# Performance work log

Hardware: AMD Instinct MI355X
Metric: run time of the kernel (lower is better)

## Reference

```python
import jax, jax.numpy as jnp
import numpy as np

N = 50000      # nodes
E = 100000     # edges
D_IN = 16      # raw node feature dim
K = 16         # RWSE steps
H = 32         # node_hidden_dim (== D_IN + K for residual)
ED = H * H     # edge_input_dim, must be H*H for NNConv reshape


def _seg_sum(x, idx, n):
    return jax.ops.segment_sum(x, idx, num_segments=n)


def setup_inputs() -> dict:
    key = jax.random.key(0)
    ks = jax.random.split(key, 14)
    s = 0.02
    return {
        "n_feat": jax.random.normal(ks[0], (N, D_IN), jnp.float32),
        "e_feat": jax.random.normal(ks[1], (E, ED), jnp.float32),
        "src": jax.random.randint(ks[2], (E,), 0, N, jnp.int32),
        "dst": jax.random.randint(ks[3], (E,), 0, N, jnp.int32),
        "edge_proj_w": jax.random.normal(ks[4], (ED, ED), jnp.float32) * s,
        "edge_proj_b": jnp.zeros((ED,), jnp.float32),
        "gate_w": jax.random.normal(ks[5], (ED, 1), jnp.float32) * s,
        "gate_b": jnp.zeros((1,), jnp.float32),
        "lin0_w": jax.random.normal(ks[6], (D_IN + K, H), jnp.float32) * s,
        "lin0_b": jnp.zeros((H,), jnp.float32),
        "conv_bias": jnp.zeros((H,), jnp.float32),
        "message_w": jax.random.normal(ks[7], (2 * H, H), jnp.float32) * s,
        "message_b": jnp.zeros((H,), jnp.float32),
        "subgraph_w": jax.random.normal(ks[8], (2 * H, H), jnp.float32) * s,
        "subgraph_b": jnp.zeros((H,), jnp.float32),
    }


def reference(n_feat, e_feat, src, dst, edge_proj_w, edge_proj_b, gate_w, gate_b,
              lin0_w, lin0_b, conv_bias, message_w, message_b, subgraph_w, subgraph_b):
    ones_e = jnp.ones((E,), n_feat.dtype)
    deg = _seg_sum(ones_e, dst, N)                 # in-degree (adj row-sum)
    degc = jnp.where(deg == 0, 1.0, deg)

    # --- RWSE (sparse equivalent of dense adj @ x recursion) ---
    x = degc
    cols = [x]
    for _ in range(K - 1):
        x = _seg_sum(x[src], dst, N) / degc
        cols.append(x)
    rwse = jnp.stack(cols, axis=1)                 # (N, K)

    nf = jnp.concatenate([n_feat, rwse], axis=-1)  # (N, D_IN+K)
    init = nf
    out = jax.nn.relu(nf @ lin0_w + lin0_b)        # (N, H)

    # --- edge-conditioned weights (EnhancedEdgeNetwork), same every step ---
    proj = jax.nn.relu(e_feat @ edge_proj_w + edge_proj_b)   # (E, H*H)
    gate = jax.nn.sigmoid(e_feat @ gate_w + gate_b)          # (E, 1)
    W = (proj * gate).reshape(E, H, H)                       # (E, H, H)

    # --- NNConv mean-aggregation message passing (num_steps//2 iters) ---
    for _ in range(3):
        msg = jnp.einsum('eh,eho->eo', out[src], W)          # gather + transform
        neigh = _seg_sum(msg, dst, N) / degc[:, None]        # scatter-mean
        m = jax.nn.relu(neigh + out + conv_bias)             # residual (identity) + bias
        out = jnp.concatenate([m, out], axis=1) @ message_w + message_b

    # --- copy_u/mean group pooling + subgraph projection ---
    group = _seg_sum(out[src], dst, N) / degc[:, None]
    out = jnp.concatenate([out, group], axis=1) @ subgraph_w + subgraph_b
    return out + init
```

## Files before the change

kernel.cpp:

```cpp
#include <hip/hip_runtime.h>
#include <hip/hip_bf16.h>

typedef unsigned short u16;
typedef unsigned int   u32;
typedef __bf16 bf16x8 __attribute__((ext_vector_type(8)));
typedef float  f32x4  __attribute__((ext_vector_type(4)));

#define AS1 __attribute__((address_space(1)))
#define AS3 __attribute__((address_space(3)))

__device__ __forceinline__ u16 f2bf(float f){
    u32 u = __float_as_uint(f);
    u32 r = u + 0x7fffu + ((u>>16)&1u);
    return (u16)(r>>16);
}
__device__ __forceinline__ float bf2f(u16 u){ return __uint_as_float(((u32)u)<<16); }

__global__ void k_deg(const int* __restrict__ dst, float* __restrict__ degb, int E){
    int e = blockIdx.x*256 + threadIdx.x;
    if (e < E) atomicAdd(&degb[dst[e]], 1.0f);
}

__global__ void k_degc(float* __restrict__ invdeg, float* __restrict__ rw0, int n){
    int v = blockIdx.x*256 + threadIdx.x;
    if (v < n){
        float c = invdeg[v];
        if (c == 0.f) c = 1.f;
        invdeg[v] = 1.f/c;
        rw0[v] = c*c;
    }
}

__global__ void k_rwse(const float* __restrict__ cur, float* __restrict__ nxt,
                       const float* __restrict__ invdeg, const int* __restrict__ src,
                       const int* __restrict__ dst, int E){
    int e = blockIdx.x*256 + threadIdx.x;
    if (e < E){
        int s = src[e];
        atomicAdd(&nxt[dst[e]], cur[s]*invdeg[s]);
    }
}

__global__ void k_finalize(const float* __restrict__ nfeat, const float* __restrict__ rw,
                           const float* __restrict__ invdeg,
                           const float* __restrict__ lw, const float* __restrict__ lb,
                           float* __restrict__ out0, int n){
    __shared__ float lwl[1024];
    __shared__ float lbl[32];
    __shared__ float nfl[8][32];
    int tid = threadIdx.x;
    for (int i = tid; i < 1024; i += 256) lwl[i] = lw[i];
    if (tid < 32) lbl[tid] = lb[tid];
    int slot = tid>>5, o = tid&31;
    int v = blockIdx.x*8 + slot;
    float nfv = 0.f;
    if (v < n){
        nfv = (o < 16) ? nfeat[(size_t)v*16 + o]
                       : rw[(size_t)(o-16)*n + v]*invdeg[v];
    }
    nfl[slot][o] = nfv;
    __syncthreads();
    if (v < n){
        float a = lbl[o];
        #pragma unroll
        for (int j = 0; j < 32; j++) a += nfl[slot][j]*lwl[j*32+o];
        out0[(size_t)v*32 + o] = a > 0.f ? a : 0.f;
    }
}

__global__ void k_transpose(const float* __restrict__ w, u16* __restrict__ wt){
    __shared__ float t[32][33];
    int bx = blockIdx.x & 31, by = blockIdx.x >> 5;
    int x = threadIdx.x & 31, y = threadIdx.x >> 5;
    #pragma unroll
    for (int i = 0; i < 32; i += 8)
        t[y+i][x] = w[(size_t)(by*32 + y + i)*1024 + bx*32 + x];
    __syncthreads();
    #pragma unroll
    for (int i = 0; i < 32; i += 8)
        wt[(size_t)(bx*32 + y + i)*1024 + by*32 + x] = f2bf(t[x][y+i]);
}

__global__ __launch_bounds__(256) void k_prep(
    const float* __restrict__ A, const float* __restrict__ gw,
    const float* __restrict__ gb, u16* __restrict__ Abf,
    float* __restrict__ gate, int E)
{
    __shared__ f32x4 gwl[256];
    const int tid = threadIdx.x;
    const int wave = tid>>6, lane = tid&63;
    gwl[tid] = ((const f32x4*)gw)[tid];
    __syncthreads();
    const int row = blockIdx.x*4 + wave;
    if (row >= E) return;
    const f32x4* ar = (const f32x4*)(A + (size_t)row*1024);
    ushort4* br = (ushort4*)(Abf + (size_t)row*1024);
    float g = 0.f;
    #pragma unroll
    for (int j = 0; j < 4; j++){
        const int idx = j*64 + lane;
        f32x4 v = ar[idx];
        f32x4 w4 = gwl[idx];
        g += v.x*w4.x + v.y*w4.y + v.z*w4.z + v.w*w4.w;
        ushort4 o;
        o.x = f2bf(v.x); o.y = f2bf(v.y); o.z = f2bf(v.z); o.w = f2bf(v.w);
        br[idx] = o;
    }
    #pragma unroll
    for (int m = 32; m >= 1; m >>= 1) g += __shfl_xor(g, m);
    if (lane == 0) gate[row] = 1.f/(1.f + __expf(-(g + gb[0])));
}

__global__ __launch_bounds__(256) void k_gemm(
    const u16* __restrict__ A, const u16* __restrict__ BT,
    const float* __restrict__ bias, const float* __restrict__ gate,
    u16* __restrict__ Wout, int E)
{
    __shared__ __align__(16) u16 lds_a[3*128*32];
    __shared__ __align__(16) u16 lds_b[3*128*32];
    __shared__ float gate_lds[128];
    __shared__ float bias_lds[128];

    const int tid  = threadIdx.x;
    const int wave = tid>>6, lane = tid&63;
    const int wm = wave>>1, wn = wave&1;
    const int ql = lane>>4, rl = lane&15;

    const int id  = blockIdx.x;
    const int xcd = id & 7;
    const int s   = id >> 3;
    const int nb  = s & 7;
    const int mb  = (s >> 3)*8 + xcd;
    const int MBtot = (E + 127) >> 7;
    if (mb >= MBtot) return;
    const int m0 = mb<<7, n0 = nb<<7;

    if (tid < 128){
        const int row = m0 + tid;
        gate_lds[tid] = gate[row < E ? row : E-1];
    } else {
        bias_lds[tid-128] = bias[n0 + tid - 128];
    }
    __syncthreads();

    const int ci0 = (0*4 + wave)*64 + lane;
    const int ci1 = (1*4 + wave)*64 + lane;
    const int mA0 = ci0>>2, cA0 = ci0&3, qA0 = cA0 ^ ((mA0>>1)&3);
    const int mA1 = ci1>>2, cA1 = ci1&3, qA1 = cA1 ^ ((mA1>>1)&3);
    int rA0 = m0 + mA0; if (rA0 >= E) rA0 = E-1;
    int rA1 = m0 + mA1; if (rA1 >= E) rA1 = E-1;
    const u16* pA0 = A + (size_t)rA0*1024 + qA0*8;
    const u16* pA1 = A + (size_t)rA1*1024 + qA1*8;
    const u16* pB0 = BT + (size_t)(n0 + mA0)*1024 + qA0*8;
    const u16* pB1 = BT + (size_t)(n0 + mA1)*1024 + qA1*8;
    const int cb0 = (0*4 + wave)*64;
    const int cb1 = (1*4 + wave)*64;

#define STAGE(buf)                                                          \
    {                                                                       \
        __builtin_amdgcn_global_load_lds((const AS1 void*)pA0,              \
            (AS3 void*)&lds_a[(buf)*4096 + cb0*8], 16, 0, 0);               \
        __builtin_amdgcn_global_load_lds((const AS1 void*)pB0,              \
            (AS3 void*)&lds_b[(buf)*4096 + cb0*8], 16, 0, 0);               \
        __builtin_amdgcn_global_load_lds((const AS1 void*)pA1,              \
            (AS3 void*)&lds_a[(buf)*4096 + cb1*8], 16, 0, 0);               \
        __builtin_amdgcn_global_load_lds((const AS1 void*)pB1,              \
            (AS3 void*)&lds_b[(buf)*4096 + cb1*8], 16, 0, 0);               \
        pA0 += 32; pA1 += 32; pB0 += 32; pB1 += 32;                         \
    }

    const int xr = (rl>>1)&3;
    const int a_off = (wm*64 + rl)*32 + (ql ^ xr)*8;
    const int b_off = (wn*64 + rl)*32 + (ql ^ xr)*8;

    f32x4 acc[4][4];
    #pragma unroll
    for (int i=0;i<4;i++)
    #pragma unroll
        for (int j=0;j<4;j++) acc[i][j] = (f32x4){0.f,0.f,0.f,0.f};

    STAGE(0)
    STAGE(1)
    asm volatile("s_waitcnt vmcnt(4)" ::: "memory");
    __builtin_amdgcn_s_barrier();

    int bc = 0;
    for (int t = 0; t < 32; ++t){
        if (t + 2 < 32){
            int bs = bc + 2; if (bs >= 3) bs -= 3;
            STAGE(bs)
        }

        const u16* la = &lds_a[bc*4096];
        const u16* lb = &lds_b[bc*4096];
        bf16x8 af[4], bfr[4];
        #pragma unroll
        for (int tt=0;tt<4;tt++){
            af[tt]  = *(const bf16x8*)&la[a_off + tt*512];
            bfr[tt] = *(const bf16x8*)&lb[b_off + tt*512];
        }
        #pragma unroll
        for (int mt=0;mt<4;mt++)
        #pragma unroll
            for (int nt=0;nt<4;nt++)
                acc[mt][nt] = __builtin_amdgcn_mfma_f32_16x16x32_bf16(af[mt], bfr[nt], acc[mt][nt], 0,0,0);

        if (t + 2 < 32)      asm volatile("s_waitcnt vmcnt(4)" ::: "memory");
        else if (t + 1 < 32) asm volatile("s_waitcnt vmcnt(0)" ::: "memory");
        if (t + 1 < 32) __builtin_amdgcn_s_barrier();

        bc = bc + 1; if (bc >= 3) bc -= 3;
    }
#undef STAGE

    float bcol[4];
    #pragma unroll
    for (int nt=0;nt<4;nt++) bcol[nt] = bias_lds[wn*64 + nt*16 + rl];

    #pragma unroll
    for (int mt=0;mt<4;mt++){
        const int rloc0 = wm*64 + mt*16 + ql*4;
        #pragma unroll
        for (int r=0;r<4;r++){
            const int row = m0 + rloc0 + r;
            if (row < E){
                const float g = gate_lds[rloc0 + r];
                u16* wrow = Wout + (size_t)row*1024 + n0 + wn*64 + rl;
                #pragma unroll
                for (int nt=0;nt<4;nt++){
                    float v = acc[mt][nt][r] + bcol[nt];
                    v = v > 0.f ? v : 0.f;
                    wrow[nt*16] = f2bf(v*g);
                }
            }
        }
    }
}

__global__ void k_msg(const float* __restrict__ outc, const u16* __restrict__ W,
                      const int* __restrict__ src, const int* __restrict__ dst,
                      float* __restrict__ neigh, int E)
{
    __shared__ float xl[8][32];
    const int tid = threadIdx.x, slot = tid>>5, o = tid&31;
    const int e = blockIdx.x*8 + slot;
    int d = 0;
    if (e < E){
        d = dst[e];
        xl[slot][o] = outc[(size_t)src[e]*32 + o];
    }
    __syncthreads();
    if (e < E){
        const float* x = xl[slot];
        const u16* wr = W + (size_t)e*1024 + o;
        float acc = 0.f;
        #pragma unroll
        for (int h = 0; h < 32; h++)
            acc += x[h]*bf2f(wr[h*32]);
        atomicAdd(&neigh[(size_t)d*32 + o], acc);
    }
}

__global__ void k_node(const float* __restrict__ neigh, const float* __restrict__ invdeg,
                       const float* __restrict__ outc, const float* __restrict__ cb,
                       const float* __restrict__ mw, const float* __restrict__ mb,
                       float* __restrict__ outn, int n)
{
    __shared__ float mwl[2048];
    __shared__ float cat[8][64];
    int tid = threadIdx.x;
    for (int i = tid; i < 2048; i += 256) mwl[i] = mw[i];
    int slot = tid>>5, o = tid&31;
    int v = blockIdx.x*8 + slot;
    if (v < n){
        float ov = outc[(size_t)v*32 + o];
        float m = neigh[(size_t)v*32 + o]*invdeg[v] + ov + cb[o];
        m = m > 0.f ? m : 0.f;
        cat[slot][o] = m;
        cat[slot][32+o] = ov;
    }
    __syncthreads();
    if (v < n){
        float a = mb[o];
        #pragma unroll
        for (int j = 0; j < 64; j++) a += cat[slot][j]*mwl[j*32+o];
        outn[(size_t)v*32 + o] = a;
    }
}

__global__ void k_group(const float* __restrict__ outc, const int* __restrict__ src,
                        const int* __restrict__ dst, float* __restrict__ grp, int E)
{
    int tid = threadIdx.x, slot = tid>>5, o = tid&31;
    int e = blockIdx.x*8 + slot;
    if (e < E)
        atomicAdd(&grp[(size_t)dst[e]*32 + o], outc[(size_t)src[e]*32 + o]);
}

__global__ void k_final(const float* __restrict__ outc, const float* __restrict__ grp,
                        const float* __restrict__ invdeg, const float* __restrict__ sw,
                        const float* __restrict__ sb, const float* __restrict__ nfeat,
                        const float* __restrict__ rw,
                        float* __restrict__ dout, int n)
{
    __shared__ float swl[2048];
    __shared__ float cat[8][64];
    int tid = threadIdx.x;
    for (int i = tid; i < 2048; i += 256) swl[i] = sw[i];
    int slot = tid>>5, o = tid&31;
    int v = blockIdx.x*8 + slot;
    float iv = 0.f;
    if (v < n){
        iv = invdeg[v];
        cat[slot][o] = outc[(size_t)v*32 + o];
        cat[slot][32+o] = grp[(size_t)v*32 + o]*iv;
    }
    __syncthreads();
    if (v < n){
        float a = sb[o];
        #pragma unroll
        for (int j = 0; j < 64; j++) a += cat[slot][j]*swl[j*32+o];
        float initv = (o < 16) ? nfeat[(size_t)v*16 + o]
                               : rw[(size_t)(o-16)*n + v]*iv;
        dout[(size_t)v*32 + o] = a + initv;
    }
}

extern "C" void kernel_launch(void* const* d_in, const int* in_sizes, int n_in,
                              void* d_out, int out_size, void* d_ws, size_t ws_size,
                              hipStream_t stream)
{
    const float* n_feat = (const float*)d_in[0];
    const float* e_feat = (const float*)d_in[1];
    const int*   src    = (const int*)d_in[2];
    const int*   dst    = (const int*)d_in[3];
    const float* epw    = (const float*)d_in[4];
    const float* epb    = (const float*)d_in[5];
    const float* gw     = (const float*)d_in[6];
    const float* gb     = (const float*)d_in[7];
    const float* l0w    = (const float*)d_in[8];
    const float* l0b    = (const float*)d_in[9];
    const float* cb     = (const float*)d_in[10];
    const float* mw     = (const float*)d_in[11];
    const float* mbp    = (const float*)d_in[12];
    const float* sw     = (const float*)d_in[13];
    const float* sb     = (const float*)d_in[14];

    const int N = in_sizes[0] / 16;
    const int E = in_sizes[2];

    char* w = (char*)d_ws;
    float* invdeg = (float*)w;  w += (size_t)N*4;
    float* rw     = (float*)w;  w += (size_t)16*N*4;
    float* out_a  = (float*)w;  w += (size_t)32*N*4;
    float* out_b  = (float*)w;  w += (size_t)32*N*4;
    float* neigh  = (float*)w;  w += (size_t)32*N*4;
    u16*   wtb    = (u16*)w;    w += (size_t)1024*1024*2;
    u16*   abf    = (u16*)w;    w += (size_t)E*1024*2;
    float* gatev  = (float*)w;  w += (size_t)E*4;
    u16*   wout   = (u16*)w;

    hipMemsetAsync(invdeg, 0, (size_t)N*4, stream);
    hipMemsetAsync(rw, 0, (size_t)16*N*4, stream);

    const int EB  = (E + 255)/256, NB = (N + 255)/256;
    const int EB8 = (E + 7)/8,    NB8 = (N + 7)/8;

    k_deg<<<EB,256,0,stream>>>(dst, invdeg, E);
    k_degc<<<NB,256,0,stream>>>(invdeg, rw, N);
    for (int t = 0; t < 15; t++)
        k_rwse<<<EB,256,0,stream>>>(rw + (size_t)t*N, rw + (size_t)(t+1)*N, invdeg, src, dst, E);
    k_finalize<<<NB8,256,0,stream>>>(n_feat, rw, invdeg, l0w, l0b, out_a, N);

    k_transpose<<<1024,256,0,stream>>>(epw, wtb);
    k_prep<<<(E+3)/4,256,0,stream>>>(e_feat, gw, gb, abf, gatev, E);

    const int MBtot = (E + 127)/128;
    const int grid  = ((MBtot + 7)/8)*64;
    k_gemm<<<grid,256,0,stream>>>(abf, wtb, epb, gatev, wout, E);

    float* cur = out_a; float* nxt = out_b;
    for (int it = 0; it < 3; it++){
        hipMemsetAsync(neigh, 0, (size_t)32*N*4, stream);
        k_msg<<<EB8,256,0,stream>>>(cur, wout, src, dst, neigh, E);
        k_node<<<NB8,256,0,stream>>>(neigh, invdeg, cur, cb, mw, mbp, nxt, N);
        float* tmp = cur; cur = nxt; nxt = tmp;
    }

    hipMemsetAsync(neigh, 0, (size_t)32*N*4, stream);
    k_group<<<EB8,256,0,stream>>>(cur, src, dst, neigh, E);
    k_final<<<NB8,256,0,stream>>>(cur, neigh, invdeg, sw, sb, n_feat, rw, (float*)d_out, N);

    (void)n_in; (void)out_size; (void)ws_size;
}
```

Measured before the change: 1.264 ms.

## Build CSR by destination and replace atomic scatters with gather-based kernels

Builds a CSR (per-destination row pointers via a single-block scan plus an atomic fill) and has the GEMM write edge weight matrices in CSR-permuted order. RWSE, message passing and group pooling become per-node gather loops instead of per-edge float atomics, and message passing is fused with the node update, removing the memsets and separate node kernels. This trades atomic contention and extra passes for a serial one-block scan, load imbalance across high-degree nodes, scattered GEMM output rows, and a 32-register accumulator with a shuffle reduction.

```diff
diff --git a/kernel.cpp b/kernel.cpp
--- a/kernel.cpp
+++ b/kernel.cpp
@@ -16,29 +16,78 @@
 }
 __device__ __forceinline__ float bf2f(u16 u){ return __uint_as_float(((u32)u)<<16); }
 
-__global__ void k_deg(const int* __restrict__ dst, float* __restrict__ degb, int E){
+__global__ void k_deg(const int* __restrict__ dst, int* __restrict__ degi, int E){
     int e = blockIdx.x*256 + threadIdx.x;
-    if (e < E) atomicAdd(&degb[dst[e]], 1.0f);
-}
-
-__global__ void k_degc(float* __restrict__ invdeg, float* __restrict__ rw0, int n){
+    if (e < E) atomicAdd(&degi[dst[e]], 1);
+}
+
+__global__ __launch_bounds__(1024) void k_scan(const int* __restrict__ degi,
+        int* __restrict__ row_ptr, int* __restrict__ cursor, int n, int E)
+{
+    __shared__ int tot[1024];
+    const int t = threadIdx.x;
+    const int per = (n + 1023) >> 10;
+    const int base = t*per;
+    int s = 0;
+    for (int i = 0; i < per; i++){
+        int idx = base + i;
+        if (idx < n) s += degi[idx];
+    }
+    tot[t] = s;
+    __syncthreads();
+    for (int off = 1; off < 1024; off <<= 1){
+        int u = (t >= off) ? tot[t-off] : 0;
+        __syncthreads();
+        tot[t] += u;
+        __syncthreads();
+    }
+    int run = tot[t] - s;
+    for (int i = 0; i < per; i++){
+        int idx = base + i;
+        if (idx < n){
+            int d = degi[idx];
+            row_ptr[idx] = run;
+            cursor[idx]  = run;
+            run += d;
+        }
+    }
+    if (t == 0) row_ptr[n] = E;
+}
+
+__global__ void k_degc(const int* __restrict__ degi, float* __restrict__ invdeg,
+                       float* __restrict__ rw0, float* __restrict__ sc0, int n){
     int v = blockIdx.x*256 + threadIdx.x;
     if (v < n){
-        float c = invdeg[v];
-        if (c == 0.f) c = 1.f;
+        int d = degi[v];
+        float c = d == 0 ? 1.f : (float)d;
         invdeg[v] = 1.f/c;
         rw0[v] = c*c;
-    }
-}
-
-__global__ void k_rwse(const float* __restrict__ cur, float* __restrict__ nxt,
-                       const float* __restrict__ invdeg, const int* __restrict__ src,
-                       const int* __restrict__ dst, int E){
+        sc0[v] = c;
+    }
+}
+
+__global__ void k_fill(const int* __restrict__ src, const int* __restrict__ dst,
+                       int* __restrict__ cursor, int* __restrict__ esrc,
+                       int* __restrict__ perm, int E){
     int e = blockIdx.x*256 + threadIdx.x;
     if (e < E){
-        int s = src[e];
-        atomicAdd(&nxt[dst[e]], cur[s]*invdeg[s]);
-    }
+        int pos = atomicAdd(&cursor[dst[e]], 1);
+        esrc[pos] = src[e];
+        perm[e] = pos;
+    }
+}
+
+__global__ void k_rwse_g(const float* __restrict__ sc_in, float* __restrict__ rw_out,
+                         float* __restrict__ sc_out, const float* __restrict__ invdeg,
+                         const int* __restrict__ row_ptr, const int* __restrict__ esrc,
+                         int n){
+    int v = blockIdx.x*256 + threadIdx.x;
+    if (v >= n) return;
+    int j0 = row_ptr[v], j1 = row_ptr[v+1];
+    float a = 0.f;
+    for (int j = j0; j < j1; j++) a += sc_in[esrc[j]];
+    rw_out[v] = a;
+    sc_out[v] = a*invdeg[v];
 }
 
 __global__ void k_finalize(const float* __restrict__ nfeat, const float* __restrict__ rw,
@@ -114,12 +163,13 @@
 __global__ __launch_bounds__(256) void k_gemm(
     const u16* __restrict__ A, const u16* __restrict__ BT,
     const float* __restrict__ bias, const float* __restrict__ gate,
-    u16* __restrict__ Wout, int E)
+    const int* __restrict__ perm, u16* __restrict__ Wout, int E)
 {
     __shared__ __align__(16) u16 lds_a[3*128*32];
     __shared__ __align__(16) u16 lds_b[3*128*32];
     __shared__ float gate_lds[128];
     __shared__ float bias_lds[128];
+    __shared__ int   perm_lds[128];
 
     const int tid  = threadIdx.x;
     const int wave = tid>>6, lane = tid&63;
@@ -137,7 +187,9 @@
 
     if (tid < 128){
         const int row = m0 + tid;
-        gate_lds[tid] = gate[row < E ? row : E-1];
+        const int cr  = row < E ? row : E-1;
+        gate_lds[tid] = gate[cr];
+        perm_lds[tid] = perm[cr];
     } else {
         bias_lds[tid-128] = bias[n0 + tid - 128];
     }
@@ -222,10 +274,11 @@
         const int rloc0 = wm*64 + mt*16 + ql*4;
         #pragma unroll
         for (int r=0;r<4;r++){
-            const int row = m0 + rloc0 + r;
+            const int rloc = rloc0 + r;
+            const int row = m0 + rloc;
             if (row < E){
-                const float g = gate_lds[rloc0 + r];
-                u16* wrow = Wout + (size_t)row*1024 + n0 + wn*64 + rl;
+                const float g = gate_lds[rloc];
+                u16* wrow = Wout + (size_t)perm_lds[rloc]*1024 + n0 + wn*64 + rl;
                 #pragma unroll
                 for (int nt=0;nt<4;nt++){
                     float v = acc[mt][nt][r] + bcol[nt];
@@ -237,93 +290,127 @@
     }
 }
 
-__global__ void k_msg(const float* __restrict__ outc, const u16* __restrict__ W,
-                      const int* __restrict__ src, const int* __restrict__ dst,
-                      float* __restrict__ neigh, int E)
-{
-    __shared__ float xl[8][32];
-    const int tid = threadIdx.x, slot = tid>>5, o = tid&31;
-    const int e = blockIdx.x*8 + slot;
-    int d = 0;
-    if (e < E){
-        d = dst[e];
-        xl[slot][o] = outc[(size_t)src[e]*32 + o];
-    }
-    __syncthreads();
-    if (e < E){
-        const float* x = xl[slot];
-        const u16* wr = W + (size_t)e*1024 + o;
-        float acc = 0.f;
-        #pragma unroll
-        for (int h = 0; h < 32; h++)
-            acc += x[h]*bf2f(wr[h*32]);
-        atomicAdd(&neigh[(size_t)d*32 + o], acc);
-    }
-}
-
-__global__ void k_node(const float* __restrict__ neigh, const float* __restrict__ invdeg,
-                       const float* __restrict__ outc, const float* __restrict__ cb,
-                       const float* __restrict__ mw, const float* __restrict__ mb,
-                       float* __restrict__ outn, int n)
+__global__ __launch_bounds__(256) void k_msgnode(
+    const float* __restrict__ outc, const u16* __restrict__ W,
+    const int* __restrict__ row_ptr, const int* __restrict__ esrc,
+    const float* __restrict__ invdeg, const float* __restrict__ cbv,
+    const float* __restrict__ mw, const float* __restrict__ mb,
+    float* __restrict__ outn, int n)
 {
     __shared__ float mwl[2048];
-    __shared__ float cat[8][64];
-    int tid = threadIdx.x;
+    const int tid = threadIdx.x;
     for (int i = tid; i < 2048; i += 256) mwl[i] = mw[i];
-    int slot = tid>>5, o = tid&31;
-    int v = blockIdx.x*8 + slot;
-    if (v < n){
-        float ov = outc[(size_t)v*32 + o];
-        float m = neigh[(size_t)v*32 + o]*invdeg[v] + ov + cb[o];
-        m = m > 0.f ? m : 0.f;
-        cat[slot][o] = m;
-        cat[slot][32+o] = ov;
-    }
-    __syncthreads();
-    if (v < n){
-        float a = mb[o];
-        #pragma unroll
-        for (int j = 0; j < 64; j++) a += cat[slot][j]*mwl[j*32+o];
-        outn[(size_t)v*32 + o] = a;
-    }
-}
-
-__global__ void k_group(const float* __restrict__ outc, const int* __restrict__ src,
-                        const int* __restrict__ dst, float* __restrict__ grp, int E)
-{
-    int tid = threadIdx.x, slot = tid>>5, o = tid&31;
-    int e = blockIdx.x*8 + slot;
-    if (e < E)
-        atomicAdd(&grp[(size_t)dst[e]*32 + o], outc[(size_t)src[e]*32 + o]);
-}
-
-__global__ void k_final(const float* __restrict__ outc, const float* __restrict__ grp,
-                        const float* __restrict__ invdeg, const float* __restrict__ sw,
-                        const float* __restrict__ sb, const float* __restrict__ nfeat,
-                        const float* __restrict__ rw,
-                        float* __restrict__ dout, int n)
+    __syncthreads();
+    const int slot = tid>>5, l = tid&31;
+    const int v = blockIdx.x*8 + slot;
+    if (v >= n) return;
+
+    const int j0 = row_ptr[v], j1 = row_ptr[v+1];
+    float acc[32];
+    #pragma unroll
+    for (int i=0;i<32;i++) acc[i] = 0.f;
+
+    for (int j = j0; j < j1; j++){
+        const int s = esrc[j];
+        const float xl = outc[(size_t)s*32 + l];
+        const uint4* wq = (const uint4*)(W + (size_t)j*1024 + l*32);
+        #pragma unroll
+        for (int c = 0; c < 4; c++){
+            uint4 q = wq[c];
+            u32 ws[4] = {q.x, q.y, q.z, q.w};
+            #pragma unroll
+            for (int k = 0; k < 4; k++){
+                float flo = __uint_as_float(ws[k] << 16);
+                float fhi = __uint_as_float(ws[k] & 0xffff0000u);
+                acc[c*8 + k*2]     += xl*flo;
+                acc[c*8 + k*2 + 1] += xl*fhi;
+            }
+        }
+    }
+
+    float r1[16], r2[8], r3[4], r4[2], msg;
+    {
+        const int b0 = l & 1;
+        #pragma unroll
+        for (int i=0;i<16;i++){
+            float keep = b0 ? acc[2*i+1] : acc[2*i];
+            float send = b0 ? acc[2*i]   : acc[2*i+1];
+            r1[i] = keep + __shfl_xor(send, 1, 32);
+        }
+        const int b1 = (l>>1)&1;
+        #pragma unroll
+        for (int i=0;i<8;i++){
+            float keep = b1 ? r1[2*i+1] : r1[2*i];
+            float send = b1 ? r1[2*i]   : r1[2*i+1];
+            r2[i] = keep + __shfl_xor(send, 2, 32);
+        }
+        const int b2 = (l>>2)&1;
+        #pragma unroll
+        for (int i=0;i<4;i++){
+            float keep = b2 ? r2[2*i+1] : r2[2*i];
+            float send = b2 ? r2[2*i]   : r2[2*i+1];
+            r3[i] = keep + __shfl_xor(send, 4, 32);
+        }
+        const int b3 = (l>>3)&1;
+        #pragma unroll
+        for (int i=0;i<2;i++){
+            float keep = b3 ? r3[2*i+1] : r3[2*i];
+            float send = b3 ? r3[2*i]   : r3[2*i+1];
+            r4[i] = keep + __shfl_xor(send, 8, 32);
+        }
+        const int b4 = (l>>4)&1;
+        {
+            float keep = b4 ? r4[1] : r4[0];
+            float send = b4 ? r4[0] : r4[1];
+            msg = keep + __shfl_xor(send, 16, 32);
+        }
+    }
+
+    const float iv = invdeg[v];
+    const float ov = outc[(size_t)v*32 + l];
+    float m = msg*iv + ov + cbv[l];
+    m = m > 0.f ? m : 0.f;
+
+    float a = mb[l];
+    #pragma unroll
+    for (int j = 0; j < 32; j++) a += __shfl(m, j, 32)*mwl[j*32 + l];
+    #pragma unroll
+    for (int j = 0; j < 32; j++) a += __shfl(ov, j, 32)*mwl[(32+j)*32 + l];
+    outn[(size_t)v*32 + l] = a;
+}
+
+__global__ __launch_bounds__(256) void k_fingroup(
+    const float* __restrict__ outc, const int* __restrict__ row_ptr,
+    const int* __restrict__ esrc, const float* __restrict__ invdeg,
+    const float* __restrict__ sw, const float* __restrict__ sb,
+    const float* __restrict__ nfeat, const float* __restrict__ rw,
+    float* __restrict__ dout, int n)
 {
     __shared__ float swl[2048];
-    __shared__ float cat[8][64];
-    int tid = threadIdx.x;
+    const int tid = threadIdx.x;
     for (int i = tid; i < 2048; i += 256) swl[i] = sw[i];
-    int slot = tid>>5, o = tid&31;
-    int v = blockIdx.x*8 + slot;
-    float iv = 0.f;
-    if (v < n){
-        iv = invdeg[v];
-        cat[slot][o] = outc[(size_t)v*32 + o];
-        cat[slot][32+o] = grp[(size_t)v*32 + o]*iv;
-    }
-    __syncthreads();
-    if (v < n){
-        float a = sb[o];
-        #pragma unroll
-        for (int j = 0; j < 64; j++) a += cat[slot][j]*swl[j*32+o];
-        float initv = (o < 16) ? nfeat[(size_t)v*16 + o]
-                               : rw[(size_t)(o-16)*n + v]*iv;
-        dout[(size_t)v*32 + o] = a + initv;
-    }
+    __syncthreads();
+    const int slot = tid>>5, l = tid&31;
+    const int v = blockIdx.x*8 + slot;
+    if (v >= n) return;
+
+    const int j0 = row_ptr[v], j1 = row_ptr[v+1];
+    float g = 0.f;
+    for (int j = j0; j < j1; j++)
+        g += outc[(size_t)esrc[j]*32 + l];
+    const float iv = invdeg[v];
+    g *= iv;
+    const float ov = outc[(size_t)v*32 + l];
+
+    float a = sb[l];
+    #pragma unroll
+    for (int j = 0; j < 32; j++) a += __shfl(ov, j, 32)*swl[j*32 + l];
+    #pragma unroll
+    for (int j = 0; j < 32; j++) a += __shfl(g,  j, 32)*swl[(32+j)*32 + l];
+
+    float initv = (l < 16) ? nfeat[(size_t)v*16 + l]
+                           : rw[(size_t)(l-16)*n + v]*iv;
+    dout[(size_t)v*32 + l] = a + initv;
 }
 
 extern "C" void kernel_launch(void* const* d_in, const int* in_sizes, int n_in,
@@ -350,26 +437,38 @@
     const int E = in_sizes[2];
 
     char* w = (char*)d_ws;
+    int*   degi   = (int*)w;    w += (size_t)N*4;
+    int*   row_ptr= (int*)w;    w += (size_t)(N+1)*4;
+    int*   cursor = (int*)w;    w += (size_t)N*4;
+    int*   esrc   = (int*)w;    w += (size_t)E*4;
+    int*   perm   = (int*)w;    w += (size_t)E*4;
     float* invdeg = (float*)w;  w += (size_t)N*4;
+    float* sc_a   = (float*)w;  w += (size_t)N*4;
+    float* sc_b   = (float*)w;  w += (size_t)N*4;
     float* rw     = (float*)w;  w += (size_t)16*N*4;
     float* out_a  = (float*)w;  w += (size_t)32*N*4;
     float* out_b  = (float*)w;  w += (size_t)32*N*4;
-    float* neigh  = (float*)w;  w += (size_t)32*N*4;
+    float* gatev  = (float*)w;  w += (size_t)E*4;
     u16*   wtb    = (u16*)w;    w += (size_t)1024*1024*2;
     u16*   abf    = (u16*)w;    w += (size_t)E*1024*2;
-    float* gatev  = (float*)w;  w += (size_t)E*4;
     u16*   wout   = (u16*)w;
 
-    hipMemsetAsync(invdeg, 0, (size_t)N*4, stream);
-    hipMemsetAsync(rw, 0, (size_t)16*N*4, stream);
+    hipMemsetAsync(degi, 0, (size_t)N*4, stream);
 
     const int EB  = (E + 255)/256, NB = (N + 255)/256;
-    const int EB8 = (E + 7)/8,    NB8 = (N + 7)/8;
-
-    k_deg<<<EB,256,0,stream>>>(dst, invdeg, E);
-    k_degc<<<NB,256,0,stream>>>(invdeg, rw, N);
-    for (int t = 0; t < 15; t++)
-        k_rwse<<<EB,256,0,stream>>>(rw + (size_t)t*N, rw + (size_t)(t+1)*N, invdeg, src, dst, E);
+    const int NB8 = (N + 7)/8;
+
+    k_deg<<<EB,256,0,stream>>>(dst, degi, E);
+    k_scan<<<1,1024,0,stream>>>(degi, row_ptr, cursor, N, E);
+    k_degc<<<NB,256,0,stream>>>(degi, invdeg, rw, sc_a, N);
+    k_fill<<<EB,256,0,stream>>>(src, dst, cursor, esrc, perm, E);
+
+    float* scur = sc_a; float* snxt = sc_b;
+    for (int t = 0; t < 15; t++){
+        k_rwse_g<<<NB,256,0,stream>>>(scur, rw + (size_t)(t+1)*N, snxt,
+                                      invdeg, row_ptr, esrc, N);
+        float* tmp = scur; scur = snxt; snxt = tmp;
+    }
     k_finalize<<<NB8,256,0,stream>>>(n_feat, rw, invdeg, l0w, l0b, out_a, N);
 
     k_transpose<<<1024,256,0,stream>>>(epw, wtb);
@@ -377,19 +476,17 @@
 
     const int MBtot = (E + 127)/128;
     const int grid  = ((MBtot + 7)/8)*64;
-    k_gemm<<<grid,256,0,stream>>>(abf, wtb, epb, gatev, wout, E);
+    k_gemm<<<grid,256,0,stream>>>(abf, wtb, epb, gatev, perm, wout, E);
 
     float* cur = out_a; float* nxt = out_b;
     for (int it = 0; it < 3; it++){
-        hipMemsetAsync(neigh, 0, (size_t)32*N*4, stream);
-        k_msg<<<EB8,256,0,stream>>>(cur, wout, src, dst, neigh, E);
-        k_node<<<NB8,256,0,stream>>>(neigh, invdeg, cur, cb, mw, mbp, nxt, N);
+        k_msgnode<<<NB8,256,0,stream>>>(cur, wout, row_ptr, esrc, invdeg,
+                                        cb, mw, mbp, nxt, N);
         float* tmp = cur; cur = nxt; nxt = tmp;
     }
 
-    hipMemsetAsync(neigh, 0, (size_t)32*N*4, stream);
-    k_group<<<EB8,256,0,stream>>>(cur, src, dst, neigh, E);
-    k_final<<<NB8,256,0,stream>>>(cur, neigh, invdeg, sw, sb, n_feat, rw, (float*)d_out, N);
+    k_fingroup<<<NB8,256,0,stream>>>(cur, row_ptr, esrc, invdeg, sw, sb,
+                                     n_feat, rw, (float*)d_out, N);
 
     (void)n_in; (void)out_size; (void)ws_size;
 }
```

New measurement: 1.408 ms. 11.4% more time.
